# Kernel tuning notes

Hardware: AMD Instinct MI355X
Metric: run time of the kernel (lower is better)

## Reference

```python
import jax, jax.numpy as jnp
import numpy as np

N_E = 1024      # codes per sub-codebook
E_DIM = 64      # code dimension
BETA = 0.25     # commitment cost (VectorQuantizer(n_e, e_dim, 0.25))


def setup_inputs() -> dict:
    key = jax.random.key(0)
    k1, k2 = jax.random.split(key)
    bs, c, h, w = 16, 512, 32, 32
    m = c // E_DIM  # 8 sub-codebooks
    z = jax.random.normal(k1, (bs, c, h, w), dtype=jnp.float32)
    # taming-style init: uniform(-1/n_e, 1/n_e)
    codebooks = jax.random.uniform(
        k2, (m, N_E, E_DIM), dtype=jnp.float32,
        minval=-1.0 / N_E, maxval=1.0 / N_E)
    return {"z": z, "codebooks": codebooks}


def reference(z, codebooks):
    bs, c, h, w = z.shape
    m, n_e, e_dim = codebooks.shape
    N = bs * h * w
    # [bs,c,h,w] -> [bs,h,w,c] -> [m, N, e_dim]: batched over all m sub-codebooks at once
    zf = z.transpose(0, 2, 3, 1).reshape(N, m, e_dim).transpose(1, 0, 2)

    # squared L2 distances: ||z||^2 + ||e||^2 - 2 z.e   -> [m, N, n_e]
    d = ((zf ** 2).sum(-1, keepdims=True)
         + (codebooks ** 2).sum(-1)[:, None, :]
         - 2.0 * jnp.einsum('mnd,mkd->mnk', zf, codebooks))
    idx = jnp.argmin(d, axis=-1)  # [m, N]

    # gather nearest codes: [m, N, e_dim]
    zq = jnp.take_along_axis(codebooks, idx[:, :, None], axis=1)

    # per-sub-codebook VQ loss, summed over m (loss = sum(loss_list))
    codebook_loss = jnp.mean((jax.lax.stop_gradient(zq) - zf) ** 2, axis=(1, 2))
    commit_loss = jnp.mean((zq - jax.lax.stop_gradient(zf)) ** 2, axis=(1, 2))
    loss = jnp.sum(codebook_loss + BETA * commit_loss)

    # straight-through estimator
    zq_st = zf + jax.lax.stop_gradient(zq - zf)

    # reassemble: [m,N,d] -> [N,m*d] -> [bs,h,w,c] -> [bs,c,h,w]
    z_vq = zq_st.transpose(1, 0, 2).reshape(bs, h, w, c).transpose(0, 3, 1, 2)

    # concat of per-codebook index tensors along dim 0
    min_encoding_indices = idx.reshape(-1)  # [m*N]
    # per-code occupancy counts summed over the m codebooks -> [n_e]
    bin_count = jnp.zeros((n_e,), jnp.int32).at[min_encoding_indices].add(1)

    return z_vq, loss, min_encoding_indices, bin_count
```

## Files before the change

### kernel.cpp

```cpp
#include <hip/hip_runtime.h>
#include <cfloat>

#define BS 16
#define CC 512
#define HWD 1024
#define NN 16384
#define MM 8
#define NE 1024
#define ED 64

#define LOSS_OFF 8388608
#define IDX_OFF  8388609
#define BIN_OFF  8519681

#define TAU 4e-5f
#define UWIN 400u

#define WS_B     0
#define WS_IDX   32768
#define WS_CNT   557056
#define WS_LIST  557088
#define WS_OF    688160
#define WS_CAND  720928
#define WS_BMAT  3866656

typedef __attribute__((ext_vector_type(8))) short bf16x8;
typedef __attribute__((ext_vector_type(16))) float f32x16;

__device__ __forceinline__ unsigned short f2bf(float f) {
    unsigned int u = __float_as_uint(f);
    unsigned int r = (u + 0x7fffu + ((u >> 16) & 1u)) >> 16;
    return (unsigned short)r;
}
__device__ __forceinline__ float bf2f(unsigned short h) {
    return __uint_as_float(((unsigned int)h) << 16);
}
__device__ __forceinline__ unsigned umin_(unsigned a, unsigned b) { return a < b ? a : b; }
__device__ __forceinline__ unsigned umax_(unsigned a, unsigned b) { return a > b ? a : b; }
__device__ __forceinline__ unsigned umin3(unsigned a, unsigned b, unsigned c) {
    return umin_(umin_(a, b), c);
}

__device__ __forceinline__ float mul_rn(float a, float b) {
#pragma clang fp contract(off)
    return a * b;
}
__device__ __forceinline__ float add_rn(float a, float b) {
#pragma clang fp contract(off)
    return a + b;
}
__device__ __forceinline__ float sub_rn(float a, float b) {
#pragma clang fp contract(off)
    return a - b;
}

__device__ __forceinline__ float np_sumsq64(const float* x) {
    float r[8];
#pragma unroll
    for (int j = 0; j < 8; ++j) r[j] = mul_rn(x[j], x[j]);
#pragma unroll
    for (int i = 8; i < 64; i += 8) {
#pragma unroll
        for (int j = 0; j < 8; ++j) r[j] = add_rn(r[j], mul_rn(x[i + j], x[i + j]));
    }
    return add_rn(add_rn(add_rn(r[0], r[1]), add_rn(r[2], r[3])),
                  add_rn(add_rn(r[4], r[5]), add_rn(r[6], r[7])));
}

__device__ __forceinline__ float np_dot64(const float* zsh, const float4* cr4) {
    float v0 = 0.f, v1 = 0.f, v2 = 0.f, v3 = 0.f;
#pragma unroll
    for (int t = 0; t < 4; ++t) {
        float4 e0 = cr4[t * 4 + 0];
        float4 e1 = cr4[t * 4 + 1];
        float4 e2 = cr4[t * 4 + 2];
        float4 e3 = cr4[t * 4 + 3];
        const int d0 = 16 * t;
        v0 = add_rn(mul_rn(zsh[d0 + 0], e0.x),
             add_rn(mul_rn(zsh[d0 + 4], e1.x),
             add_rn(mul_rn(zsh[d0 + 8], e2.x),
             add_rn(mul_rn(zsh[d0 + 12], e3.x), v0))));
        v1 = add_rn(mul_rn(zsh[d0 + 1], e0.y),
             add_rn(mul_rn(zsh[d0 + 5], e1.y),
             add_rn(mul_rn(zsh[d0 + 9], e2.y),
             add_rn(mul_rn(zsh[d0 + 13], e3.y), v1))));
        v2 = add_rn(mul_rn(zsh[d0 + 2], e0.z),
             add_rn(mul_rn(zsh[d0 + 6], e1.z),
             add_rn(mul_rn(zsh[d0 + 10], e2.z),
             add_rn(mul_rn(zsh[d0 + 14], e3.z), v2))));
        v3 = add_rn(mul_rn(zsh[d0 + 3], e0.w),
             add_rn(mul_rn(zsh[d0 + 7], e1.w),
             add_rn(mul_rn(zsh[d0 + 11], e2.w),
             add_rn(mul_rn(zsh[d0 + 15], e3.w), v3))));
    }
    return add_rn(add_rn(v0, v1), add_rn(v2, v3));
}

__global__ __launch_bounds__(256) void prep_kernel(const float* __restrict__ cb,
                                                   float* __restrict__ Bhat,
                                                   uint4* __restrict__ Bmat,
                                                   float* __restrict__ out,
                                                   int* __restrict__ cnt) {
    const int tid = threadIdx.x;
    if (blockIdx.x < 32) {
        int i = blockIdx.x * 256 + tid;
        if (i == 0) { out[LOSS_OFF] = 0.0f; cnt[0] = 0; cnt[1] = 0; }
        if (i < NE) out[BIN_OFF + i] = 0.0f;
        const float4* r4 = (const float4*)(cb + (size_t)i * ED);
        float x[ED];
#pragma unroll
        for (int q = 0; q < 16; ++q) {
            float4 v = r4[q];
            x[q*4+0] = v.x; x[q*4+1] = v.y; x[q*4+2] = v.z; x[q*4+3] = v.w;
        }
        Bhat[i] = np_sumsq64(x);
        return;
    }
    int t = (blockIdx.x - 32) * 256 + tid;
    int lane = t & 63;
    int ct = (t >> 6) & 31;
    int rem = t >> 11;
    int c = rem % 13;
    int m = rem / 13;
    int h = lane >> 5;
    int k = ct * 32 + (lane & 31);

    unsigned short v[8];
#pragma unroll
    for (int j = 0; j < 8; ++j) v[j] = 0;

    if (c < 12) {
        int d0 = 16 * (c & 3) + 8 * h;
        const float* e = cb + ((size_t)m * NE + k) * ED + d0;
#pragma unroll
        for (int j = 0; j < 8; ++j) {
            float f = -2.0f * e[j];
            unsigned short hi = f2bf(f);
            v[j] = (c >= 4 && c < 8) ? f2bf(f - bf2f(hi)) : hi;
        }
    } else if (h == 0) {
        const float* e = cb + ((size_t)m * NE + k) * ED;
        float s = 0.f;
#pragma unroll
        for (int d = 0; d < ED; ++d) s += e[d] * e[d];
        v[0] = f2bf(s);
        v[1] = 0x3F80;
    }
    uint4 o;
    o.x = (unsigned)v[0] | ((unsigned)v[1] << 16);
    o.y = (unsigned)v[2] | ((unsigned)v[3] << 16);
    o.z = (unsigned)v[4] | ((unsigned)v[5] << 16);
    o.w = (unsigned)v[6] | ((unsigned)v[7] << 16);
    Bmat[t] = o;
}

__global__ __launch_bounds__(512, 4) void argmin_kernel(
        const float* __restrict__ z, const uint4* __restrict__ Bmat,
        int* __restrict__ idx_out, int* __restrict__ cnt,
        int* __restrict__ list, unsigned short* __restrict__ cand) {
    const int tid = threadIdx.x;
    const int m = blockIdx.y;
    const int row0 = blockIdx.x * 256;
    const int w = tid >> 6;
    const int l = tid & 63;
    const int h = l >> 5;
    const int r5 = l & 31;

    __shared__ uint4 ldsB[3][13 * 2 * 64];

    const int n_mine = row0 + w * 32 + r5;
    const int b = n_mine >> 10;
    const int hw = n_mine & (HWD - 1);
    const float* zbase = z + (((size_t)(b * CC + m * ED)) << 10) + hw;

    bf16x8 zh[4], zl[4];
#pragma unroll
    for (int i = 0; i < 4; ++i) {
        int o = 2 * i + h;
#pragma unroll
        for (int j = 0; j < 8; ++j) {
            float f = zbase[(size_t)(8 * o + j) << 10];
            unsigned short hb = f2bf(f);
            unsigned short lb = f2bf(f - bf2f(hb));
            zh[i][j] = (short)hb;
            zl[i][j] = (short)lb;
        }
    }
    bf16x8 ones12 = {0, 0, 0, 0, 0, 0, 0, 0};
    if (h == 0) { ones12[0] = (short)0x3F80; ones12[1] = (short)0x3F80; }

    unsigned rbm = 0xFFFFFFF0u, rsec = 0xFFFFFFFFu, rinfo = 0;
    int ccnt = 0;
    unsigned cq0 = 0, cq1 = 0, cq2 = 0;
    auto push = [&](unsigned id) {
        cq2 = (cq2 << 16) | (cq1 >> 16);
        cq1 = (cq1 << 16) | (cq0 >> 16);
        cq0 = (cq0 << 16) | (id & 0xFFFFu);
        ccnt++;
    };

    auto stage = [&](int g, int bufi) {
        for (int seg = w; seg < 26; seg += 8) {
            int c = seg >> 1, ct2 = seg & 1;
            const uint4* src = Bmat +
                ((size_t)((m * 13 + c) * 32 + (g * 2 + ct2)) << 6) + l;
            uint4* dst = &ldsB[bufi][(c * 2 + ct2) * 64];
            __builtin_amdgcn_global_load_lds(
                (const __attribute__((address_space(1))) unsigned int*)src,
                (__attribute__((address_space(3))) unsigned int*)dst, 16, 0, 0);
        }
    };

    auto process = [&](const f32x16& acc, unsigned tile) {
        unsigned u[16];
#pragma unroll
        for (int s = 0; s < 16; ++s)
            u[s] = (__float_as_uint(acc[s]) & 0xFFFFFFF0u) | (unsigned)s;
        unsigned b0 = umin_(u[0], u[1]),  s0 = umax_(u[0], u[1]);
        unsigned b1 = umin_(u[2], u[3]),  s1 = umax_(u[2], u[3]);
        unsigned b2 = umin_(u[4], u[5]),  s2 = umax_(u[4], u[5]);
        unsigned b3 = umin_(u[6], u[7]),  s3 = umax_(u[6], u[7]);
        unsigned b4 = umin_(u[8], u[9]),  s4 = umax_(u[8], u[9]);
        unsigned b5 = umin_(u[10], u[11]), s5 = umax_(u[10], u[11]);
        unsigned b6 = umin_(u[12], u[13]), s6 = umax_(u[12], u[13]);
        unsigned b7 = umin_(u[14], u[15]), s7 = umax_(u[14], u[15]);
        unsigned B0 = umin_(b0, b1), S0 = umin3(umax_(b0, b1), s0, s1);
        unsigned B1 = umin_(b2, b3), S1 = umin3(umax_(b2, b3), s2, s3);
        unsigned B2 = umin_(b4, b5), S2 = umin3(umax_(b4, b5), s4, s5);
        unsigned B3 = umin_(b6, b7), S3 = umin3(umax_(b6, b7), s6, s7);
        unsigned C0 = umin_(B0, B1), T0 = umin3(umax_(B0, B1), S0, S1);
        unsigned C1 = umin_(B2, B3), T1 = umin3(umax_(B2, B3), S2, S3);
        unsigned bt = umin_(C0, C1), st = umin3(umax_(C0, C1), T0, T1);

        unsigned oldrbm = rbm;
        bool take = bt < oldrbm;
        unsigned newrbm = take ? bt : oldrbm;
        unsigned limit = newrbm + UWIN;
        rsec = umin3(rsec, st, take ? oldrbm : bt);
        int sbt = (int)(bt & 15u);
        if (take) {
            if (bt + UWIN < oldrbm) ccnt = 0;
            push(tile * 32u + ((unsigned)sbt & 3u) +
                 8u * ((unsigned)sbt >> 2) + 4u * (unsigned)h);
            rinfo = (tile << 4) | (unsigned)sbt;
        }
        rbm = newrbm;
        unsigned gatev = take ? st : bt;
        if (gatev < limit) {
#pragma unroll
            for (int s = 0; s < 16; ++s) {
                if (u[s] < limit && !(take && s == sbt))
                    push(tile * 32u + ((unsigned)s & 3u) +
                         8u * ((unsigned)s >> 2) + 4u * (unsigned)h);
            }
        }
    };

    stage(0, 0);
    stage(1, 1);
    asm volatile("s_waitcnt vmcnt(3)" ::: "memory");
    __builtin_amdgcn_s_barrier();

    int bR = 0;
    for (int g = 0; g < 16; ++g) {
        int bW = bR + 2; if (bW >= 3) bW -= 3;
        if (g < 14) stage(g + 2, bW);
        const uint4* Bb = &ldsB[bR][0];

        f32x16 a0, a1;
#pragma unroll
        for (int s = 0; s < 16; ++s) { a0[s] = 0.0f; a1[s] = 0.0f; }
        __builtin_amdgcn_s_setprio(1);
#pragma unroll
        for (int c = 0; c < 13; ++c) {
            bf16x8 af0 = *(const bf16x8*)&Bb[(c * 2 + 0) * 64 + l];
            bf16x8 af1 = *(const bf16x8*)&Bb[(c * 2 + 1) * 64 + l];
            bf16x8 zf = (c < 8) ? zh[c & 3] : ((c < 12) ? zl[c & 3] : ones12);
            a0 = __builtin_amdgcn_mfma_f32_32x32x16_bf16(af0, zf, a0, 0, 0, 0);
            a1 = __builtin_amdgcn_mfma_f32_32x32x16_bf16(af1, zf, a1, 0, 0, 0);
        }
        __builtin_amdgcn_s_setprio(0);
        process(a0, (unsigned)(g * 2 + 0));
        process(a1, (unsigned)(g * 2 + 1));

        if (g < 14) {
            asm volatile("s_waitcnt vmcnt(3)" ::: "memory");
        } else if (g == 14) {
            asm volatile("s_waitcnt vmcnt(0)" ::: "memory");
        }
        if (g < 15) __builtin_amdgcn_s_barrier();
        bR = (bR == 2) ? 0 : bR + 1;
    }

    unsigned short* myslots = cand + ((size_t)(m * NN + n_mine) * 2 + h) * 6;
    if (ccnt) {
        unsigned* cp = (unsigned*)myslots;
        cp[0] = cq0; cp[1] = cq1; cp[2] = cq2;
    }

    int pcnt = __shfl_xor(ccnt, 32, 64);

    unsigned ss = rinfo & 15u, tile = rinfo >> 4;
    int k = (int)(tile * 32 + (ss & 3u) + 8u * (ss >> 2) + 4u * (unsigned)h);
    unsigned orbm = __shfl_xor(rbm, 32, 64);
    int ok = __shfl_xor(k, 32, 64);
    unsigned orsec = __shfl_xor(rsec, 32, 64);
    bool take = orbm < rbm;
    unsigned lose = take ? rbm : orbm;
    unsigned fb = take ? orbm : rbm;
    int fk = take ? ok : k;
    unsigned fs = umin3(rsec, orsec, lose);
    if (l < 32) {
        int mn = m * NN + n_mine;
        idx_out[mn] = fk;
        float margin = __uint_as_float(fs & 0xFFFFFFF0u) -
                       __uint_as_float(fb & 0xFFFFFFF0u);
        if (margin < TAU) {
            int p = atomicAdd(cnt, 1);
            if (p < 32768) {
                int c0 = ccnt > 6 ? 7 : ccnt;
                int c1 = pcnt > 6 ? 7 : pcnt;
                list[p] = mn | (c0 << 20) | (c1 << 24);
            }
        }
    }
}

__global__ __launch_bounds__(256) void cand_kernel(
        const float* __restrict__ z, const float* __restrict__ cb,
        const float* __restrict__ Bhat, int* __restrict__ cnt,
        const int* __restrict__ list, const unsigned short* __restrict__ cand,
        int* __restrict__ idx_out, int* __restrict__ oflist) {
    const int tid = threadIdx.x;
    const int lane = tid & 63;
    const int wv = tid >> 6;
    const int wid = (blockIdx.x * 256 + tid) >> 6;
    const int nw = gridDim.x * 4;
    const int total = cnt[0] < 32768 ? cnt[0] : 32768;

    __shared__ float zsh[4][ED];

    for (int r = wid; r < total; r += nw) {
        const int e = list[r];
        const int mn = e & 0xFFFFF;
        const int c0 = (e >> 20) & 15;
        const int c1 = (e >> 24) & 15;
        if (c0 == 7 || c1 == 7) {
            if (lane == 0) {
                int q = atomicAdd(cnt + 1, 1);
                if (q < 8192) oflist[q] = mn;
            }
            continue;
        }
        const int m = mn >> 14;
        const int n = mn & (NN - 1);
        const int b = n >> 10;
        const int hw = n & (HWD - 1);

        zsh[wv][lane] = z[(((size_t)(b * CC + m * ED + lane)) << 10) + hw];

        int kj = -1;
        if (lane < c0) kj = cand[(size_t)mn * 12 + lane];
        else if (lane >= 8 && lane < 8 + c1) kj = cand[(size_t)mn * 12 + 6 + (lane - 8)];

        float A = np_sumsq64(&zsh[wv][0]);

        float dref = FLT_MAX;
        if (kj >= 0) {
            const float4* cr4 = (const float4*)(cb + ((size_t)m * NE + kj) * ED);
            float C = np_dot64(&zsh[wv][0], cr4);
            dref = sub_rn(add_rn(A, Bhat[m * NE + kj]), mul_rn(2.0f, C));
        }
        int kk = (kj >= 0) ? kj : NE;
#pragma unroll
        for (int off = 32; off >= 1; off >>= 1) {
            float ov = __shfl_down(dref, off, 64);
            int oi = __shfl_down(kk, off, 64);
            if (ov < dref || (ov == dref && oi < kk)) { dref = ov; kk = oi; }
        }
        if (lane == 0) idx_out[mn] = kk;
    }
}

__global__ __launch_bounds__(256) void emul_kernel(
        const float* __restrict__ z, const float* __restrict__ cb,
        const float* __restrict__ Bhat, const int* __restrict__ cnt,
        const int* __restrict__ oflist, int* __restrict__ idx_out) {
    const int tid = threadIdx.x;
    const int lane = tid & 63;
    const int w = tid >> 6;
    const int total = cnt[1] < 8192 ? cnt[1] : 8192;

    __shared__ float zsh[ED];
    __shared__ float rbest[4];
    __shared__ int ridx[4];

    for (int r = blockIdx.x; r < total; r += gridDim.x) {
        const int mn = oflist[r];
        const int m = mn >> 14;
        const int n = mn & (NN - 1);
        const int b = n >> 10;
        const int hw = n & (HWD - 1);

        __syncthreads();
        if (tid < ED) {
            const float* zbase = z + (((size_t)(b * CC + m * ED)) << 10) + hw;
            zsh[tid] = zbase[(size_t)tid << 10];
        }
        __syncthreads();

        const float A = np_sumsq64(zsh);
        const float* cbm = cb + (size_t)m * NE * ED;
        const float* Bm = Bhat + m * NE;
        float best = FLT_MAX;
        int bidx = NE;
#pragma unroll
        for (int kk = 0; kk < 4; ++kk) {
            const int k = kk * 256 + tid;
            const float4* cr4 = (const float4*)(cbm + (size_t)k * ED);
            float C = np_dot64(zsh, cr4);
            float dk = sub_rn(add_rn(A, Bm[k]), mul_rn(2.0f, C));
            if (dk < best || (dk == best && k < bidx)) { best = dk; bidx = k; }
        }
#pragma unroll
        for (int off = 32; off >= 1; off >>= 1) {
            float ov = __shfl_down(best, off, 64);
            int oi = __shfl_down(bidx, off, 64);
            if (ov < best || (ov == best && oi < bidx)) { best = ov; bidx = oi; }
        }
        if (lane == 0) { rbest[w] = best; ridx[w] = bidx; }
        __syncthreads();
        if (tid == 0) {
            float bb = rbest[0]; int bi = ridx[0];
#pragma unroll
            for (int i = 1; i < 4; ++i) {
                if (rbest[i] < bb || (rbest[i] == bb && ridx[i] < bi)) {
                    bb = rbest[i]; bi = ridx[i];
                }
            }
            idx_out[mn] = bi;
        }
    }
}

__global__ __launch_bounds__(256) void output_kernel(
        const float* __restrict__ z, const float* __restrict__ cb,
        const int* __restrict__ idx_in, float* __restrict__ out) {
    const int tid = threadIdx.x;
    const int n = blockIdx.x * 256 + tid;
    const int m = blockIdx.y;
    const int b = n >> 10;
    const int hw = n & (HWD - 1);
    const int idx = idx_in[m * NN + n];

    out[IDX_OFF + m * NN + n] = (float)idx;

    const float* cr = cb + ((size_t)m * NE + (size_t)idx) * ED;
    const float* zbase = z + (((size_t)(b * CC + m * ED)) << 10) + hw;
    float* ob = out + (((size_t)(b * CC + m * ED)) << 10) + hw;

    double acc = 0.0;
#pragma unroll
    for (int d = 0; d < ED; ++d) {
        float c = cr[d];
        float zv = zbase[(size_t)d << 10];
        ob[(size_t)d << 10] = c;
        float diff = c - zv;
        acc += (double)diff * (double)diff;
    }

    __shared__ int hist[NE];
#pragma unroll
    for (int i = 0; i < 4; ++i) hist[tid + i * 256] = 0;
    __syncthreads();
    atomicAdd(&hist[idx], 1);

#pragma unroll
    for (int off = 32; off >= 1; off >>= 1)
        acc += __shfl_down(acc, off, 64);
    __shared__ double wsum[4];
    if ((tid & 63) == 0) wsum[tid >> 6] = acc;
    __syncthreads();
    if (tid == 0) {
        double t = wsum[0] + wsum[1] + wsum[2] + wsum[3];
        atomicAdd(out + LOSS_OFF, (float)(t * (1.25 / 1048576.0)));
    }
#pragma unroll
    for (int i = 0; i < 4; ++i) {
        int v = hist[tid + i * 256];
        if (v) atomicAdd(out + BIN_OFF + tid + i * 256, (float)v);
    }
}

extern "C" void kernel_launch(void* const* d_in, const int* in_sizes, int n_in,
                              void* d_out, int out_size, void* d_ws, size_t ws_size,
                              hipStream_t stream) {
    const float* z = (const float*)d_in[0];
    const float* cb = (const float*)d_in[1];
    float* out = (float*)d_out;
    char* ws = (char*)d_ws;
    float* Bhat = (float*)(ws + WS_B);
    int* idxw = (int*)(ws + WS_IDX);
    int* cnt = (int*)(ws + WS_CNT);
    int* list = (int*)(ws + WS_LIST);
    int* oflist = (int*)(ws + WS_OF);
    unsigned short* cand = (unsigned short*)(ws + WS_CAND);
    uint4* Bmat = (uint4*)(ws + WS_BMAT);

    prep_kernel<<<dim3(864), dim3(256), 0, stream>>>(cb, Bhat, Bmat, out, cnt);
    argmin_kernel<<<dim3(NN / 256, MM), dim3(512), 0, stream>>>(
        z, Bmat, idxw, cnt, list, cand);
    cand_kernel<<<dim3(256), dim3(256), 0, stream>>>(
        z, cb, Bhat, cnt, list, cand, idxw, oflist);
    emul_kernel<<<dim3(256), dim3(256), 0, stream>>>(
        z, cb, Bhat, cnt, oflist, idxw);
    output_kernel<<<dim3(NN / 256, MM), dim3(256), 0, stream>>>(z, cb, idxw, out);
}
```

Measured before the change: 179.9 us.

## Software-pipeline MFMA chains with candidate processing using double accumulators

Restructures the main codebook-tile loop so the MFMA chain for the next tile runs interleaved with processing (argmin candidate filtering) of the previous tile's accumulators, using two ping-pong accumulator sets. The goal is to hide the latency of the VALU-heavy process step behind matrix-core work instead of serializing them. In exchange it uses more accumulator registers, which may raise register pressure or reduce occupancy, and the loop is unrolled by two, making the code larger.

```diff
diff --git a/kernel.cpp b/kernel.cpp
--- a/kernel.cpp
+++ b/kernel.cpp
@@ -256,41 +256,81 @@
         }
     };
 
+    auto zero2 = [&](f32x16& x0, f32x16& x1) {
+#pragma unroll
+        for (int s = 0; s < 16; ++s) { x0[s] = 0.0f; x1[s] = 0.0f; }
+    };
+    auto mchain = [&](f32x16& x0, f32x16& x1, const uint4* Bb, int c0, int c1) {
+        __builtin_amdgcn_s_setprio(1);
+#pragma unroll
+        for (int c = c0; c < c1; ++c) {
+            bf16x8 af0 = *(const bf16x8*)&Bb[(c * 2 + 0) * 64 + l];
+            bf16x8 af1 = *(const bf16x8*)&Bb[(c * 2 + 1) * 64 + l];
+            bf16x8 zf = (c < 8) ? zh[c & 3] : ((c < 12) ? zl[c & 3] : ones12);
+            x0 = __builtin_amdgcn_mfma_f32_32x32x16_bf16(af0, zf, x0, 0, 0, 0);
+            x1 = __builtin_amdgcn_mfma_f32_32x32x16_bf16(af1, zf, x1, 0, 0, 0);
+        }
+        __builtin_amdgcn_s_setprio(0);
+    };
+
+    f32x16 A0, A1, B0, B1;
+
     stage(0, 0);
     stage(1, 1);
     asm volatile("s_waitcnt vmcnt(3)" ::: "memory");
     __builtin_amdgcn_s_barrier();
 
-    int bR = 0;
-    for (int g = 0; g < 16; ++g) {
-        int bW = bR + 2; if (bW >= 3) bW -= 3;
-        if (g < 14) stage(g + 2, bW);
-        const uint4* Bb = &ldsB[bR][0];
-
-        f32x16 a0, a1;
-#pragma unroll
-        for (int s = 0; s < 16; ++s) { a0[s] = 0.0f; a1[s] = 0.0f; }
-        __builtin_amdgcn_s_setprio(1);
-#pragma unroll
-        for (int c = 0; c < 13; ++c) {
-            bf16x8 af0 = *(const bf16x8*)&Bb[(c * 2 + 0) * 64 + l];
-            bf16x8 af1 = *(const bf16x8*)&Bb[(c * 2 + 1) * 64 + l];
-            bf16x8 zf = (c < 8) ? zh[c & 3] : ((c < 12) ? zl[c & 3] : ones12);
-            a0 = __builtin_amdgcn_mfma_f32_32x32x16_bf16(af0, zf, a0, 0, 0, 0);
-            a1 = __builtin_amdgcn_mfma_f32_32x32x16_bf16(af1, zf, a1, 0, 0, 0);
-        }
-        __builtin_amdgcn_s_setprio(0);
-        process(a0, (unsigned)(g * 2 + 0));
-        process(a1, (unsigned)(g * 2 + 1));
-
-        if (g < 14) {
+    stage(2, 2);
+    zero2(A0, A1);
+    mchain(A0, A1, &ldsB[0][0], 0, 13);
+    asm volatile("s_waitcnt vmcnt(3)" ::: "memory");
+    __builtin_amdgcn_s_barrier();
+
+    for (int gg = 0; gg < 7; ++gg) {
+        const int g1 = 2 * gg + 1;
+        stage(g1 + 2, (g1 + 2) % 3);
+        {
+            const uint4* Bb = &ldsB[g1 % 3][0];
+            zero2(B0, B1);
+            mchain(B0, B1, Bb, 0, 5);
+            process(A0, (unsigned)(2 * g1 - 2));
+            mchain(B0, B1, Bb, 5, 9);
+            process(A1, (unsigned)(2 * g1 - 1));
+            mchain(B0, B1, Bb, 9, 13);
+        }
+        asm volatile("s_waitcnt vmcnt(3)" ::: "memory");
+        __builtin_amdgcn_s_barrier();
+
+        const int g2 = 2 * gg + 2;
+        if (g2 < 14) stage(g2 + 2, (g2 + 2) % 3);
+        {
+            const uint4* Bb = &ldsB[g2 % 3][0];
+            zero2(A0, A1);
+            mchain(A0, A1, Bb, 0, 5);
+            process(B0, (unsigned)(2 * g2 - 2));
+            mchain(A0, A1, Bb, 5, 9);
+            process(B1, (unsigned)(2 * g2 - 1));
+            mchain(A0, A1, Bb, 9, 13);
+        }
+        if (g2 < 14) {
             asm volatile("s_waitcnt vmcnt(3)" ::: "memory");
-        } else if (g == 14) {
+        } else {
             asm volatile("s_waitcnt vmcnt(0)" ::: "memory");
         }
-        if (g < 15) __builtin_amdgcn_s_barrier();
-        bR = (bR == 2) ? 0 : bR + 1;
-    }
+        __builtin_amdgcn_s_barrier();
+    }
+
+    {
+        const uint4* Bb = &ldsB[0][0];
+        zero2(B0, B1);
+        mchain(B0, B1, Bb, 0, 5);
+        process(A0, 28u);
+        mchain(B0, B1, Bb, 5, 9);
+        process(A1, 29u);
+        mchain(B0, B1, Bb, 9, 13);
+    }
+    process(B0, 30u);
+    process(B1, 31u);
 
     unsigned short* myslots = cand + ((size_t)(m * NN + n_mine) * 2 + h) * 6;
     if (ccnt) {
```

Result: slower. 188.4 us (+4.7%).

## Software-pipeline MFMA chains with candidate processing and stagger wave priority

Applied to the files above, without the earlier changes.

Restructures the main codebook-tile loop so that the scalar/VALU processing of the previous accumulator tile is interleaved between halves of the next MFMA chains, instead of running two full MFMA chains then processing both. The first tile group is peeled and the final tile processed after the loop. Only odd waves raise their scheduling priority, letting waves alternate between matrix and vector phases. This aims to overlap MFMA latency with the argmin/candidate bookkeeping, at the cost of holding an extra accumulator (more VGPRs) and more complex control flow.

```diff
diff --git a/kernel.cpp b/kernel.cpp
--- a/kernel.cpp
+++ b/kernel.cpp
@@ -256,33 +256,55 @@
         }
     };
 
+    auto zero1 = [&](f32x16& x) {
+#pragma unroll
+        for (int s = 0; s < 16; ++s) x[s] = 0.0f;
+    };
+    auto chain = [&](f32x16& x, const uint4* Bb, int ctl, int c0, int c1) {
+#pragma unroll
+        for (int c = c0; c < c1; ++c) {
+            bf16x8 af = *(const bf16x8*)&Bb[(c * 2 + ctl) * 64 + l];
+            bf16x8 zf = (c < 8) ? zh[c & 3] : ((c < 12) ? zl[c & 3] : ones12);
+            x = __builtin_amdgcn_mfma_f32_32x32x16_bf16(af, zf, x, 0, 0, 0);
+        }
+    };
+
+    f32x16 C0, C1, P;
+    const bool hiprio = (w & 1) != 0;
+
     stage(0, 0);
     stage(1, 1);
     asm volatile("s_waitcnt vmcnt(3)" ::: "memory");
     __builtin_amdgcn_s_barrier();
 
-    int bR = 0;
-    for (int g = 0; g < 16; ++g) {
-        int bW = bR + 2; if (bW >= 3) bW -= 3;
-        if (g < 14) stage(g + 2, bW);
+    stage(2, 2);
+    if (hiprio) __builtin_amdgcn_s_setprio(1);
+    zero1(C0);
+    chain(C0, &ldsB[0][0], 0, 0, 13);
+    zero1(C1);
+    chain(C1, &ldsB[0][0], 1, 0, 6);
+    process(C0, 0u);
+    chain(C1, &ldsB[0][0], 1, 6, 13);
+    P = C1;
+    if (hiprio) __builtin_amdgcn_s_setprio(0);
+    asm volatile("s_waitcnt vmcnt(3)" ::: "memory");
+    __builtin_amdgcn_s_barrier();
+
+    int bR = 1;
+    for (int g = 1; g < 16; ++g) {
+        if (g < 14) stage(g + 2, (g + 2) % 3);
         const uint4* Bb = &ldsB[bR][0];
-
-        f32x16 a0, a1;
-#pragma unroll
-        for (int s = 0; s < 16; ++s) { a0[s] = 0.0f; a1[s] = 0.0f; }
-        __builtin_amdgcn_s_setprio(1);
-#pragma unroll
-        for (int c = 0; c < 13; ++c) {
-            bf16x8 af0 = *(const bf16x8*)&Bb[(c * 2 + 0) * 64 + l];
-            bf16x8 af1 = *(const bf16x8*)&Bb[(c * 2 + 1) * 64 + l];
-            bf16x8 zf = (c < 8) ? zh[c & 3] : ((c < 12) ? zl[c & 3] : ones12);
-            a0 = __builtin_amdgcn_mfma_f32_32x32x16_bf16(af0, zf, a0, 0, 0, 0);
-            a1 = __builtin_amdgcn_mfma_f32_32x32x16_bf16(af1, zf, a1, 0, 0, 0);
-        }
-        __builtin_amdgcn_s_setprio(0);
-        process(a0, (unsigned)(g * 2 + 0));
-        process(a1, (unsigned)(g * 2 + 1));
-
+        if (hiprio) __builtin_amdgcn_s_setprio(1);
+        zero1(C0);
+        chain(C0, Bb, 0, 0, 6);
+        process(P, (unsigned)(2 * g - 1));
+        chain(C0, Bb, 0, 6, 13);
+        zero1(C1);
+        chain(C1, Bb, 1, 0, 6);
+        process(C0, (unsigned)(2 * g));
+        chain(C1, Bb, 1, 6, 13);
+        P = C1;
+        if (hiprio) __builtin_amdgcn_s_setprio(0);
         if (g < 14) {
             asm volatile("s_waitcnt vmcnt(3)" ::: "memory");
         } else if (g == 14) {
@@ -291,6 +313,7 @@
         if (g < 15) __builtin_amdgcn_s_barrier();
         bR = (bR == 2) ? 0 : bR + 1;
     }
+    process(P, 31u);
 
     unsigned short* myslots = cand + ((size_t)(m * NN + n_mine) * 2 + h) * 6;
     if (ccnt) {
```

Result: faster. 175.0 us (-2.7%).

## Load codebook fragments directly from global memory instead of LDS triple-buffering

Applied to the files above, without the earlier changes.

Removes the shared-memory triple-buffered staging of the packed codebook matrix, which used global_load_lds, vmcnt waits and block-wide barriers. Each wave now reads its MFMA operand fragments straight from global memory (L2/L1-resident) with a two-deep register prefetch inside the K loop. This drops the LDS footprint and the per-iteration barriers, which may raise occupancy and decouple the waves. In exchange, every wave issues its own redundant global loads and load latency is only partially hidden by the short prefetch distance.

```diff
diff --git a/kernel.cpp b/kernel.cpp
--- a/kernel.cpp
+++ b/kernel.cpp
@@ -166,8 +166,6 @@
     const int h = l >> 5;
     const int r5 = l & 31;
 
-    __shared__ uint4 ldsB[3][13 * 2 * 64];
-
     const int n_mine = row0 + w * 32 + r5;
     const int b = n_mine >> 10;
     const int hw = n_mine & (HWD - 1);
@@ -197,18 +195,6 @@
         cq1 = (cq1 << 16) | (cq0 >> 16);
         cq0 = (cq0 << 16) | (id & 0xFFFFu);
         ccnt++;
-    };
-
-    auto stage = [&](int g, int bufi) {
-        for (int seg = w; seg < 26; seg += 8) {
-            int c = seg >> 1, ct2 = seg & 1;
-            const uint4* src = Bmat +
-                ((size_t)((m * 13 + c) * 32 + (g * 2 + ct2)) << 6) + l;
-            uint4* dst = &ldsB[bufi][(c * 2 + ct2) * 64];
-            __builtin_amdgcn_global_load_lds(
-                (const __attribute__((address_space(1))) unsigned int*)src,
-                (__attribute__((address_space(3))) unsigned int*)dst, 16, 0, 0);
-        }
     };
 
     auto process = [&](const f32x16& acc, unsigned tile) {
@@ -256,40 +242,37 @@
         }
     };
 
-    stage(0, 0);
-    stage(1, 1);
-    asm volatile("s_waitcnt vmcnt(3)" ::: "memory");
-    __builtin_amdgcn_s_barrier();
-
-    int bR = 0;
+    const uint4* bm = Bmat + (((size_t)m * 13) << 11) + l;
+
     for (int g = 0; g < 16; ++g) {
-        int bW = bR + 2; if (bW >= 3) bW -= 3;
-        if (g < 14) stage(g + 2, bW);
-        const uint4* Bb = &ldsB[bR][0];
+        const uint4* bg = bm + ((size_t)(g * 2) << 6);
+
+        bf16x8 A0[2], A1[2];
+        A0[0] = *(const bf16x8*)(bg);
+        A1[0] = *(const bf16x8*)(bg + 64);
+        A0[1] = *(const bf16x8*)(bg + (1 << 11));
+        A1[1] = *(const bf16x8*)(bg + (1 << 11) + 64);
 
         f32x16 a0, a1;
 #pragma unroll
         for (int s = 0; s < 16; ++s) { a0[s] = 0.0f; a1[s] = 0.0f; }
+
         __builtin_amdgcn_s_setprio(1);
 #pragma unroll
         for (int c = 0; c < 13; ++c) {
-            bf16x8 af0 = *(const bf16x8*)&Bb[(c * 2 + 0) * 64 + l];
-            bf16x8 af1 = *(const bf16x8*)&Bb[(c * 2 + 1) * 64 + l];
+            bf16x8 f0 = A0[c & 1];
+            bf16x8 f1 = A1[c & 1];
+            if (c + 2 < 13) {
+                A0[c & 1] = *(const bf16x8*)(bg + ((size_t)(c + 2) << 11));
+                A1[c & 1] = *(const bf16x8*)(bg + ((size_t)(c + 2) << 11) + 64);
+            }
             bf16x8 zf = (c < 8) ? zh[c & 3] : ((c < 12) ? zl[c & 3] : ones12);
-            a0 = __builtin_amdgcn_mfma_f32_32x32x16_bf16(af0, zf, a0, 0, 0, 0);
-            a1 = __builtin_amdgcn_mfma_f32_32x32x16_bf16(af1, zf, a1, 0, 0, 0);
+            a0 = __builtin_amdgcn_mfma_f32_32x32x16_bf16(f0, zf, a0, 0, 0, 0);
+            a1 = __builtin_amdgcn_mfma_f32_32x32x16_bf16(f1, zf, a1, 0, 0, 0);
         }
         __builtin_amdgcn_s_setprio(0);
         process(a0, (unsigned)(g * 2 + 0));
         process(a1, (unsigned)(g * 2 + 1));
-
-        if (g < 14) {
-            asm volatile("s_waitcnt vmcnt(3)" ::: "memory");
-        } else if (g == 14) {
-            asm volatile("s_waitcnt vmcnt(0)" ::: "memory");
-        }
-        if (g < 15) __builtin_amdgcn_s_barrier();
-        bR = (bR == 2) ? 0 : bR + 1;
     }
 
     unsigned short* myslots = cand + ((size_t)(m * NN + n_mine) * 2 + h) * 6;
```

After: 198.0 us. 10.1% more time.
